# Performance work log

Measured on AMD Instinct MI355X. Metric: run time of the kernel, lower is better.

Reference implementation:

```python
import jax, jax.numpy as jnp
import numpy as np

B, S, H = 2, 2048, 2304
NH, HD, NKV = 8, 256, 4
WINDOW = 512
CAP = 50.0
THETA = 10000.0
NEG_INF = -2.3819763e38


def setup_inputs() -> dict:
    key = jax.random.key(0)
    ks = jax.random.split(key, 6)
    hidden_states = jax.random.normal(ks[0], (B, S, H), dtype=jnp.float32)
    # causal additive mask (0 where attend, -inf-ish where masked)
    i = jnp.arange(S)
    causal = i[None, :] <= i[:, None]
    attention_mask = jnp.broadcast_to(
        jnp.where(causal, 0.0, NEG_INF).astype(jnp.float32)[None, None], (B, 1, S, S)
    )
    position_ids = jnp.broadcast_to(jnp.arange(S, dtype=jnp.int32)[None], (B, S))
    scale = 0.02
    Wq = jax.random.normal(ks[1], (H, NH * HD), dtype=jnp.float32) * scale
    Wk = jax.random.normal(ks[2], (H, NKV * HD), dtype=jnp.float32) * scale
    Wv = jax.random.normal(ks[3], (H, NKV * HD), dtype=jnp.float32) * scale
    Wo = jax.random.normal(ks[4], (NH * HD, H), dtype=jnp.float32) * scale
    return {
        "hidden_states": hidden_states,
        "attention_mask": attention_mask,
        "position_ids": position_ids,
        "Wq": Wq,
        "Wk": Wk,
        "Wv": Wv,
        "Wo": Wo,
    }


def _rotate_half(x):
    h = x.shape[-1] // 2
    return jnp.concatenate([-x[..., h:], x[..., :h]], axis=-1)


def reference(hidden_states, attention_mask, position_ids, Wq, Wk, Wv, Wo):
    b, s, _ = hidden_states.shape
    q = (hidden_states @ Wq).reshape(b, s, NH, HD).transpose(0, 2, 1, 3)   # [B,NH,S,HD]
    k = (hidden_states @ Wk).reshape(b, s, NKV, HD).transpose(0, 2, 1, 3)  # [B,NKV,S,HD]
    v = (hidden_states @ Wv).reshape(b, s, NKV, HD).transpose(0, 2, 1, 3)
    # rotary embedding
    inv_freq = 1.0 / (THETA ** (jnp.arange(0, HD, 2, dtype=jnp.float32) / HD))
    freqs = position_ids.astype(jnp.float32)[..., None] * inv_freq  # [B,S,HD/2]
    emb = jnp.concatenate([freqs, freqs], axis=-1)                  # [B,S,HD]
    cos = jnp.cos(emb)[:, None]  # unsqueeze head dim
    sin = jnp.sin(emb)[:, None]
    q = q * cos + _rotate_half(q) * sin
    k = k * cos + _rotate_half(k) * sin
    # GQA: repeat kv heads
    rep = NH // NKV
    k = jnp.repeat(k, rep, axis=1)
    v = jnp.repeat(v, rep, axis=1)
    logits = jnp.einsum("bhqd,bhkd->bhqk", q, k) / jnp.sqrt(jnp.float32(HD))
    # sliding-window mask: keep |i-j| <= WINDOW-1, else NEG_INF
    idx = jnp.arange(s)
    sliding = jnp.abs(idx[:, None] - idx[None, :]) <= (WINDOW - 1)
    mask = jnp.where(sliding[None, None], attention_mask, NEG_INF)
    # tanh logit softcapping, then additive mask
    logits = jnp.tanh(logits / CAP) * CAP + mask
    probs = jax.nn.softmax(logits.astype(jnp.float32), axis=-1).astype(q.dtype)
    out = jnp.einsum("bhqk,bhkd->bhqd", probs, v)
    out = out.transpose(0, 2, 1, 3).reshape(b, s, NH * HD)
    return out @ Wo
```

## Files before the change

### kernel.cpp

```cpp
#include <hip/hip_runtime.h>
#include <cmath>

#define B_   2
#define S_   2048
#define H_   2304
#define NH_  8
#define HD_  256
#define NKV_ 4
#define WIN_ 512
#define QKVW 4096

typedef unsigned short ushort_t;
typedef __attribute__((ext_vector_type(8))) short bf16x8;
typedef __attribute__((ext_vector_type(4))) float floatx4;

__device__ __forceinline__ unsigned short f2bf(float f) {
  unsigned u = __builtin_bit_cast(unsigned, f);
  u += 0x7fff + ((u >> 16) & 1);
  return (unsigned short)(u >> 16);
}
__device__ __forceinline__ float bf2f(ushort_t v) {
  unsigned u = (unsigned)v << 16;
  return __builtin_bit_cast(float, u);
}

__device__ __forceinline__ void gl2lds16(const void* g, void* l) {
  __builtin_amdgcn_global_load_lds(
      (const __attribute__((address_space(1))) unsigned int*)g,
      (__attribute__((address_space(3))) unsigned int*)l, 16, 0, 0);
}

__global__ void cast_bf16(const float* __restrict__ in, ushort_t* __restrict__ out) {
  const int i = blockIdx.x * 256 + threadIdx.x;
  float4 v = ((const float4*)in)[i];
  ushort4 o;
  o.x = f2bf(v.x); o.y = f2bf(v.y); o.z = f2bf(v.z); o.w = f2bf(v.w);
  ((ushort4*)out)[i] = o;
}

__global__ void transpose_cast(const float* __restrict__ W, ushort_t* __restrict__ Wt,
                               int K, int N) {
  __shared__ float t[32][33];
  const int lx = threadIdx.x & 31, ly = threadIdx.x >> 5;
  const int n0 = blockIdx.x * 32, k0 = blockIdx.y * 32;
#pragma unroll
  for (int i = 0; i < 4; ++i)
    t[ly + i * 8][lx] = W[(long long)(k0 + ly + i * 8) * N + n0 + lx];
  __syncthreads();
#pragma unroll
  for (int i = 0; i < 4; ++i)
    Wt[(long long)(n0 + ly + i * 8) * K + k0 + lx] = f2bf(t[lx][ly + i * 8]);
}

#define RA(dst_, base_, qm_, kk_) do { \
  _Pragma("unroll") for (int i_ = 0; i_ < 4; ++i_) { \
    const int row_ = wm + (qm_) * 64 + i_ * 16 + l15; \
    dst_[i_] = *(const bf16x8*)&(base_)[row_ * 64 + ((((kk_) * 4 + lq) ^ (l15 & 7)) * 8)]; \
  } \
} while (0)

#define RB(dst_, base_, qn_, kk_) do { \
  _Pragma("unroll") for (int j_ = 0; j_ < 2; ++j_) { \
    const int row_ = wn + (qn_) * 32 + j_ * 16 + l15; \
    dst_[j_] = *(const bf16x8*)&(base_)[row_ * 64 + ((((kk_) * 4 + lq) ^ (l15 & 7)) * 8)]; \
  } \
} while (0)

#define MFMA8(qm_, qn_, as_, bs_) do { \
  __builtin_amdgcn_s_setprio(1); \
  _Pragma("unroll") for (int i_ = 0; i_ < 4; ++i_) \
  _Pragma("unroll") for (int j_ = 0; j_ < 2; ++j_) \
    acc[(qm_) * 4 + i_][(qn_) * 2 + j_] = __builtin_amdgcn_mfma_f32_16x16x32_bf16( \
        as_[i_], bs_[j_], acc[(qm_) * 4 + i_][(qn_) * 2 + j_], 0, 0, 0); \
  __builtin_amdgcn_s_setprio(0); \
} while (0)

#define STAGE_A(dst_, gsrc_, t_, qm_) do { \
  _Pragma("unroll") for (int jj_ = 0; jj_ < 2; ++jj_) { \
    const int g_ = w * 2 + jj_; \
    const int tr0_ = ((g_ >> 3) * 128) + (qm_) * 64 + (g_ & 7) * 8; \
    gl2lds16(gsrc_ + (size_t)tr0_ * K + (size_t)(t_) * 64 + laneOff, dst_ + tr0_ * 64); \
  } \
} while (0)

#define STAGE_B(dst_, gsrc_, t_, qn_) do { \
  _Pragma("unroll") for (int jj_ = 0; jj_ < 2; ++jj_) { \
    const int g_ = w * 2 + jj_; \
    const int tr0_ = ((g_ >> 2) * 64) + (qn_) * 32 + (g_ & 3) * 8; \
    gl2lds16(gsrc_ + (size_t)tr0_ * K + (size_t)(t_) * 64 + laneOff, dst_ + tr0_ * 64); \
  } \
} while (0)

#define SB0()  __builtin_amdgcn_sched_barrier(0)
#define BAR()  asm volatile("s_barrier" ::: "memory")
#define VM(n_) asm volatile("s_waitcnt vmcnt(" #n_ ")" ::: "memory")

#define KTILE(XA_, XB_, YA_, YB_, t_) do { \
   \
  RB(b1, XB_, 1, 0); \
  if ((t_) + 1 < NT) STAGE_A(YA_, Ab, (t_) + 1, 1); \
  MFMA8(0, 0, a0, b0); SB0(); \
   \
  RA(a1, XA_, 1, 0); \
  MFMA8(0, 1, a0, b1); SB0(); \
   \
  RA(a0, XA_, 1, 1); \
  MFMA8(1, 1, a1, b1); SB0(); \
   \
  RB(b1, XB_, 0, 1); \
  MFMA8(1, 0, a1, b0); SB0(); \
   \
  RB(b0, XB_, 1, 1); \
  MFMA8(1, 0, a0, b1); SB0(); BAR(); \
   \
  RA(a1, XA_, 0, 1); \
  if ((t_) + 2 < NT) STAGE_B(XB_, Bb, (t_) + 2, 0); \
  MFMA8(1, 1, a0, b0); \
  if ((t_) + 2 < NT) { VM(2); } else if ((t_) + 1 < NT) { VM(0); } \
  SB0(); BAR(); \
   \
  if ((t_) + 1 < NT) RA(a0, YA_, 0, 0); \
  if ((t_) + 2 < NT) STAGE_B(XB_, Bb, (t_) + 2, 1); \
  MFMA8(0, 1, a1, b0); SB0(); BAR(); \
   \
  if ((t_) + 1 < NT) RB(b0, YB_, 0, 0); \
  if ((t_) + 2 < NT) STAGE_A(XA_, Ab, (t_) + 2, 0); \
  MFMA8(0, 0, a1, b1); SB0(); \
} while (0)

template <bool OUT_BF16>
__launch_bounds__(512)
__global__ void gemm_8ph(const ushort_t* __restrict__ A,
                         const ushort_t* __restrict__ Bt,
                         void* __restrict__ Cv, int M, int N, int K) {
  extern __shared__ __attribute__((aligned(128))) ushort_t smem[];
  const int tid = threadIdx.x, lane = tid & 63, w = tid >> 6;
  const int wm = (w >> 2) * 128, wn = (w & 3) * 64;
  const int l15 = lane & 15, lq = lane >> 4;

  const int nwg  = gridDim.x * gridDim.y;
  const int orig = blockIdx.y * gridDim.x + blockIdx.x;
  const int cpx  = nwg >> 3;
  const int swz  = (orig & 7) * cpx + (orig >> 3);
  const int bx   = swz % gridDim.x, by = swz / gridDim.x;
  const int bm = by * 256, bn = bx * 256;
  const int NT = K >> 6;

  const ushort_t* Ab = A + (size_t)bm * K;
  const ushort_t* Bb = Bt + (size_t)bn * K;
  const size_t laneOff = (size_t)(lane >> 3) * K + (size_t)(((lane & 7) ^ (lane >> 3)) * 8);

  ushort_t* Ae = smem;
  ushort_t* Ao = smem + 16384;
  ushort_t* Be = smem + 32768;
  ushort_t* Bo = smem + 49152;

  floatx4 acc[8][4] = {};
  bf16x8 a0[4], a1[4], b0[2], b1[2];

  STAGE_A(Ae, Ab, 0, 0);
  STAGE_B(Be, Bb, 0, 0);
  STAGE_B(Be, Bb, 0, 1);
  STAGE_A(Ae, Ab, 0, 1);
  if (NT > 1) {
    STAGE_B(Bo, Bb, 1, 0);
    STAGE_B(Bo, Bb, 1, 1);
    STAGE_A(Ao, Ab, 1, 0);
    VM(6);
  } else {
    VM(0);
  }
  BAR();
  RA(a0, Ae, 0, 0);
  RB(b0, Be, 0, 0);

  for (int t = 0; t < NT; t += 2) {
    KTILE(Ae, Be, Ao, Bo, t);
    KTILE(Ao, Bo, Ae, Be, t + 1);
  }

  const int r0 = lq * 4;
#pragma unroll
  for (int mf = 0; mf < 8; ++mf)
#pragma unroll
    for (int nf = 0; nf < 4; ++nf) {
      const long long base = (long long)(bm + wm + mf * 16 + r0) * N + bn + wn + nf * 16 + l15;
      if (OUT_BF16) {
        ushort_t* Cp = (ushort_t*)Cv + base;
#pragma unroll
        for (int rr = 0; rr < 4; ++rr) Cp[(long long)rr * N] = f2bf(acc[mf][nf][rr]);
      } else {
        float* Cp = (float*)Cv + base;
#pragma unroll
        for (int rr = 0; rr < 4; ++rr) Cp[(long long)rr * N] = acc[mf][nf][rr];
      }
    }
}

#undef RA
#undef RB
#undef MFMA8
#undef STAGE_A
#undef STAGE_B
#undef SB0
#undef BAR
#undef VM
#undef KTILE

template <bool OUT_BF16>
__launch_bounds__(256)
__global__ void gemm_bt(const ushort_t* __restrict__ A,
                        const ushort_t* __restrict__ Bt,
                        void* __restrict__ Cv, int M, int N, int K) {
  __shared__ ushort_t As[128 * 64];
  __shared__ ushort_t Bs[128 * 64];
  const int tid = threadIdx.x, lane = tid & 63, wid = tid >> 6;
  const int bm = blockIdx.y * 128, bn = blockIdx.x * 128;
  const int wm = (wid >> 1) * 64, wn = (wid & 1) * 64;

  floatx4 acc[4][4] = {};

  const int r  = tid >> 1;
  const int cp = (tid & 1) * 4;
  const int wkey = r & 7;
  const ushort_t* Ap = A  + (long long)(bm + r) * K + cp * 8;
  const ushort_t* Bp = Bt + (long long)(bn + r) * K + cp * 8;
  ushort_t* Aw = &As[r * 64];
  ushort_t* Bw = &Bs[r * 64];

  const int l15 = lane & 15, lq = lane >> 4;
  const int rkey = l15 & 7;

  bf16x8 ar[4], br[4];
#pragma unroll
  for (int i = 0; i < 4; ++i) {
    ar[i] = *(const bf16x8*)(Ap + i * 8);
    br[i] = *(const bf16x8*)(Bp + i * 8);
  }

  for (int k0 = 0; k0 < K; k0 += 64) {
    __syncthreads();
#pragma unroll
    for (int i = 0; i < 4; ++i) {
      *(bf16x8*)&Aw[((cp + i) ^ wkey) * 8] = ar[i];
      *(bf16x8*)&Bw[((cp + i) ^ wkey) * 8] = br[i];
    }
    __syncthreads();

    if (k0 + 64 < K) {
      const int kn = k0 + 64;
#pragma unroll
      for (int i = 0; i < 4; ++i) {
        ar[i] = *(const bf16x8*)(Ap + kn + i * 8);
        br[i] = *(const bf16x8*)(Bp + kn + i * 8);
      }
    }

#pragma unroll
    for (int kk = 0; kk < 2; ++kk) {
      bf16x8 af[4], bfr[4];
#pragma unroll
      for (int i = 0; i < 4; ++i) {
        af[i]  = *(const bf16x8*)&As[(wm + i * 16 + l15) * 64 + ((kk * 4 + lq) ^ rkey) * 8];
        bfr[i] = *(const bf16x8*)&Bs[(wn + i * 16 + l15) * 64 + ((kk * 4 + lq) ^ rkey) * 8];
      }
#pragma unroll
      for (int i = 0; i < 4; ++i)
#pragma unroll
        for (int j = 0; j < 4; ++j)
          acc[i][j] = __builtin_amdgcn_mfma_f32_16x16x32_bf16(af[i], bfr[j], acc[i][j], 0, 0, 0);
    }
  }

  const int r0 = lq * 4, c0 = l15;
#pragma unroll
  for (int i = 0; i < 4; ++i)
#pragma unroll
    for (int j = 0; j < 4; ++j) {
      const long long base = (long long)(bm + wm + i * 16 + r0) * N + bn + wn + j * 16 + c0;
      if (OUT_BF16) {
        ushort_t* Cp = (ushort_t*)Cv + base;
#pragma unroll
        for (int rr = 0; rr < 4; ++rr) Cp[(long long)rr * N] = f2bf(acc[i][j][rr]);
      } else {
        float* Cp = (float*)Cv + base;
#pragma unroll
        for (int rr = 0; rr < 4; ++rr) Cp[(long long)rr * N] = acc[i][j][rr];
      }
    }
}

__global__ void rope_inplace(ushort_t* __restrict__ QKV16, const int* __restrict__ pos) {
  const int bs  = blockIdx.x;
  const int gid = blockIdx.y * 256 + threadIdx.x;
  const int head = gid >> 7;
  const int d    = gid & 127;
  const float pp   = (float)pos[bs];
  const float invf = __expf(-(float)d * (9.210340371976184f / 128.0f));
  const float ang  = pp * invf;
  float sn, cc;
  __sincosf(ang, &sn, &cc);
  ushort_t* base = QKV16 + (size_t)bs * QKVW + head * HD_;
  const float x1 = bf2f(base[d]);
  const float x2 = bf2f(base[d + 128]);
  float o1 = x1 * cc - x2 * sn;
  float o2 = x2 * cc + x1 * sn;
  if (head < NH_) { o1 *= 0.0625f; o2 *= 0.0625f; }
  base[d]       = f2bf(o1);
  base[d + 128] = f2bf(o2);
}

__global__ void v_prep(const ushort_t* __restrict__ QKV16, ushort_t* __restrict__ Vt16) {
  __shared__ ushort_t tile[32][33];
  const int k0 = blockIdx.x * 32, d0 = blockIdx.y * 32;
  const int b = blockIdx.z >> 2, hk = blockIdx.z & 3;
  const int lx = threadIdx.x & 31, ly = threadIdx.x >> 5;
#pragma unroll
  for (int i = 0; i < 4; ++i)
    tile[ly + 8 * i][lx] =
        QKV16[(size_t)(b * S_ + k0 + ly + 8 * i) * QKVW + 3072 + hk * HD_ + d0 + lx];
  __syncthreads();
#pragma unroll
  for (int i = 0; i < 4; ++i)
    Vt16[((size_t)(b * NKV_ + hk) * HD_ + d0 + ly + 8 * i) * S_ + k0 + lx] =
        tile[lx][ly + 8 * i];
}

__launch_bounds__(512)
__global__ void attn_mfma(const ushort_t* __restrict__ QKV16,
                          const ushort_t* __restrict__ Vt16,
                          ushort_t* __restrict__ AOb) {
  __shared__ ushort_t Ks[32 * 256];
  __shared__ ushort_t Vts[256 * 32];
  __shared__ ushort_t Ps[8][16 * 32];
  __shared__ float rsb[8][16];

  const int lane = threadIdx.x & 63, w = threadIdx.x >> 6;
  const int l15 = lane & 15, lq = lane >> 4;
  const int qb = blockIdx.x * 64;
  const int hp = blockIdx.y, b = blockIdx.z;
  const int h  = hp * 2 + (w >> 2);
  const int hw = w & 3;

  const ushort_t* Qh = QKV16 + (size_t)b * S_ * QKVW + h * HD_;
  const ushort_t* Kh = QKV16 + (size_t)b * S_ * QKVW + 2048 + hp * HD_;
  const ushort_t* Vh = Vt16 + ((size_t)(b * NKV_ + hp) * HD_) * S_;

  const int qw = qb + hw * 16;

  bf16x8 afq[8];
  {
    const ushort_t* qr = Qh + (size_t)(qw + l15) * QKVW + lq * 8;
#pragma unroll
    for (int kd = 0; kd < 8; ++kd) afq[kd] = *(const bf16x8*)(qr + kd * 32);
  }

  floatx4 acc[16] = {};
  float rs[4] = {0.f, 0.f, 0.f, 0.f};

  int kb0 = qb - (WIN_ - 1);
  if (kb0 < 0) kb0 = 0;
  kb0 &= ~31;

  const int ksp = lane & 31, ksr = lane >> 5;
  const int vsp = lane & 3,  vsr = lane >> 2;

  for (int kb = kb0; kb < qb + 64; kb += 32) {
    __syncthreads();
#pragma unroll
    for (int i = 0; i < 2; ++i) {
      const int kl = w * 4 + 2 * i + ksr;
      gl2lds16(Kh + (size_t)(kb + kl) * QKVW + (ksp ^ (kl & 31)) * 8,
               &Ks[(w * 4 + 2 * i) * 256]);
    }
#pragma unroll
    for (int i = 0; i < 2; ++i) {
      const int dl = w * 32 + 16 * i + vsr;
      gl2lds16(Vh + (size_t)dl * S_ + kb + (vsp ^ ((dl >> 1) & 3)) * 8,
               &Vts[(w * 32 + 16 * i) * 32]);
    }
    __syncthreads();

    if (kb <= qw + 15 && kb + 31 >= qw - (WIN_ - 1)) {
      ushort_t* Pw = Ps[w];
#pragma unroll
      for (int kt = 0; kt < 2; ++kt) {
        floatx4 sacc = {};
        const int keyl = kt * 16 + l15;
        const int krow = keyl * 256;
        const int ksw = keyl & 31;
#pragma unroll
        for (int kd = 0; kd < 8; ++kd) {
          bf16x8 bk = *(const bf16x8*)&Ks[krow + ((kd * 4 + lq) ^ ksw) * 8];
          sacc = __builtin_amdgcn_mfma_f32_16x16x32_bf16(afq[kd], bk, sacc, 0, 0, 0);
        }
        const int keyg = kb + keyl;
#pragma unroll
        for (int rr = 0; rr < 4; ++rr) {
          const int qg = qw + lq * 4 + rr;
          const float t = __expf(sacc[rr] * 0.04f);
          const float L = 50.f - __fdividef(100.f, t + 1.f);
          float p = __expf(L);
          p = (keyg <= qg && keyg >= qg - (WIN_ - 1)) ? p : 0.f;
          rs[rr] += p;
          const int ql = lq * 4 + rr;
          const int ch = kt * 2 + (l15 >> 3);
          Pw[ql * 32 + ((ch ^ ((ql >> 1) & 3)) * 8) + (l15 & 7)] = f2bf(p);
        }
      }
      asm volatile("s_waitcnt lgkmcnt(0)" ::: "memory");

      const bf16x8 bp = *(const bf16x8*)&Pw[l15 * 32 + ((lq ^ ((l15 >> 1) & 3)) * 8)];
      const int vsw = (l15 >> 1) & 3;
#pragma unroll
      for (int t = 0; t < 16; ++t) {
        bf16x8 av = *(const bf16x8*)&Vts[(t * 16 + l15) * 32 + ((lq ^ vsw) * 8)];
        acc[t] = __builtin_amdgcn_mfma_f32_16x16x32_bf16(av, bp, acc[t], 0, 0, 0);
      }
    }
  }

#pragma unroll
  for (int rr = 0; rr < 4; ++rr) {
    rs[rr] += __shfl_xor(rs[rr], 1, 64);
    rs[rr] += __shfl_xor(rs[rr], 2, 64);
    rs[rr] += __shfl_xor(rs[rr], 4, 64);
    rs[rr] += __shfl_xor(rs[rr], 8, 64);
  }
  if (l15 == 0) {
#pragma unroll
    for (int rr = 0; rr < 4; ++rr) rsb[w][lq * 4 + rr] = rs[rr];
  }
  asm volatile("s_waitcnt lgkmcnt(0)" ::: "memory");
  __builtin_amdgcn_wave_barrier();
  const float inv = 1.0f / rsb[w][l15];

  const size_t ob = ((size_t)(b * S_ + qw + l15) * NH_ + h) * HD_;
#pragma unroll
  for (int t = 0; t < 16; ++t) {
    ushort4 o;
    o.x = f2bf(acc[t][0] * inv);
    o.y = f2bf(acc[t][1] * inv);
    o.z = f2bf(acc[t][2] * inv);
    o.w = f2bf(acc[t][3] * inv);
    *(ushort4*)&AOb[ob + t * 16 + lq * 4] = o;
  }
}

extern "C" void kernel_launch(void* const* d_in, const int* in_sizes, int n_in,
                              void* d_out, int out_size, void* d_ws, size_t ws_size,
                              hipStream_t stream) {
  const float* X   = (const float*)d_in[0];
  const int*   pos = (const int*)d_in[2];
  const float* Wq  = (const float*)d_in[3];
  const float* Wk  = (const float*)d_in[4];
  const float* Wv  = (const float*)d_in[5];
  const float* Wo  = (const float*)d_in[6];
  float* out = (float*)d_out;

  const int M  = B_ * S_;
  const int NQ = NH_ * HD_;
  const int NK = NKV_ * HD_;

  char* w = (char*)d_ws;
  ushort_t* QKV16 = (ushort_t*)w;  w += (size_t)M * QKVW * 2;
  ushort_t* Xb    = (ushort_t*)w;  w += (size_t)M * H_ * 2;
  ushort_t* Wqkvt = (ushort_t*)w;  w += (size_t)QKVW * H_ * 2;
  ushort_t* Wot   = (ushort_t*)w;  w += (size_t)H_ * NQ * 2;
  ushort_t* Vt16  = (ushort_t*)w;  w += (size_t)B_ * NKV_ * S_ * HD_ * 2;
  ushort_t* AOb   = (ushort_t*)w;  w += (size_t)M * NQ * 2;

  static bool g_init = false, g_8ph_ok = false;
  if (!g_init) {
    hipError_t e1 = hipFuncSetAttribute(
        reinterpret_cast<const void*>(&gemm_8ph<true>),
        hipFuncAttributeMaxDynamicSharedMemorySize, 131072);
    g_8ph_ok = (e1 == hipSuccess);
    g_init = true;
  }

  dim3 blk(256);

  cast_bf16<<<(M * H_) / 1024, blk, 0, stream>>>(X, Xb);
  transpose_cast<<<dim3(NQ / 32, H_ / 32), blk, 0, stream>>>(Wq, Wqkvt, H_, NQ);
  transpose_cast<<<dim3(NK / 32, H_ / 32), blk, 0, stream>>>(Wk, Wqkvt + (size_t)2048 * H_, H_, NK);
  transpose_cast<<<dim3(NK / 32, H_ / 32), blk, 0, stream>>>(Wv, Wqkvt + (size_t)3072 * H_, H_, NK);
  transpose_cast<<<dim3(H_ / 32, NQ / 32), blk, 0, stream>>>(Wo, Wot, NQ, H_);

  if (g_8ph_ok) {
    gemm_8ph<true><<<dim3(QKVW / 256, M / 256), dim3(512), 131072, stream>>>(
        Xb, Wqkvt, QKV16, M, QKVW, H_);
  } else {
    gemm_bt<true><<<dim3(QKVW / 128, M / 128), blk, 0, stream>>>(Xb, Wqkvt, QKV16, M, QKVW, H_);
  }

  rope_inplace<<<dim3(M, 6), blk, 0, stream>>>(QKV16, pos);
  v_prep<<<dim3(S_ / 32, HD_ / 32, B_ * NKV_), blk, 0, stream>>>(QKV16, Vt16);

  attn_mfma<<<dim3(S_ / 64, NKV_, B_), dim3(512), 0, stream>>>(QKV16, Vt16, AOb);

  gemm_bt<false><<<dim3(H_ / 128, M / 128), blk, 0, stream>>>(AOb, Wot, out, M, H_, NQ);
}
```

Before: 349.1 us.

## Restructure QKV GEMM into triple-buffered 32-wide K tiles with staggered wave groups

The 256x256 QKV GEMM now uses K tiles of 32 instead of 64, with three LDS buffers in place of two. Global-to-LDS prefetch runs two tiles ahead. The two halves of the workgroup run the MFMA quadrants in opposite orders, so their LDS reads and MFMA bursts interleave. LDS use drops from 128KB to 96KB, and the phase-specific waits are replaced by a single vmcnt(0) plus barrier per tile. The cost is twice as many barrier and full-wait points per unit of K, which may reduce latency hiding.

```diff
diff --git a/kernel.cpp b/kernel.cpp
--- a/kernel.cpp
+++ b/kernel.cpp
@@ -52,17 +52,17 @@
     Wt[(long long)(n0 + ly + i * 8) * K + k0 + lx] = f2bf(t[lx][ly + i * 8]);
 }
 
-#define RA(dst_, base_, qm_, kk_) do { \
+#define RA32(dst_, base_, qm_) do { \
   _Pragma("unroll") for (int i_ = 0; i_ < 4; ++i_) { \
     const int row_ = wm + (qm_) * 64 + i_ * 16 + l15; \
-    dst_[i_] = *(const bf16x8*)&(base_)[row_ * 64 + ((((kk_) * 4 + lq) ^ (l15 & 7)) * 8)]; \
+    dst_[i_] = *(const bf16x8*)&(base_)[row_ * 32 + ((lq ^ (row_ & 3)) * 8)]; \
   } \
 } while (0)
 
-#define RB(dst_, base_, qn_, kk_) do { \
+#define RB32(dst_, base_, qn_) do { \
   _Pragma("unroll") for (int j_ = 0; j_ < 2; ++j_) { \
     const int row_ = wn + (qn_) * 32 + j_ * 16 + l15; \
-    dst_[j_] = *(const bf16x8*)&(base_)[row_ * 64 + ((((kk_) * 4 + lq) ^ (l15 & 7)) * 8)]; \
+    dst_[j_] = *(const bf16x8*)&(base_)[row_ * 32 + ((lq ^ (row_ & 3)) * 8)]; \
   } \
 } while (0)
 
@@ -75,57 +75,51 @@
   __builtin_amdgcn_s_setprio(0); \
 } while (0)
 
-#define STAGE_A(dst_, gsrc_, t_, qm_) do { \
-  _Pragma("unroll") for (int jj_ = 0; jj_ < 2; ++jj_) { \
-    const int g_ = w * 2 + jj_; \
-    const int tr0_ = ((g_ >> 3) * 128) + (qm_) * 64 + (g_ & 7) * 8; \
-    gl2lds16(gsrc_ + (size_t)tr0_ * K + (size_t)(t_) * 64 + laneOff, dst_ + tr0_ * 64); \
-  } \
-} while (0)
-
-#define STAGE_B(dst_, gsrc_, t_, qn_) do { \
-  _Pragma("unroll") for (int jj_ = 0; jj_ < 2; ++jj_) { \
-    const int g_ = w * 2 + jj_; \
-    const int tr0_ = ((g_ >> 2) * 64) + (qn_) * 32 + (g_ & 3) * 8; \
-    gl2lds16(gsrc_ + (size_t)tr0_ * K + (size_t)(t_) * 64 + laneOff, dst_ + tr0_ * 64); \
-  } \
+#define STG32(dst_, gsrc_, t_, hf_) do { \
+  const int r0_ = (hf_) * 128 + w * 16; \
+  gl2lds16(gsrc_ + (size_t)r0_ * K + (size_t)(t_) * 32 + laneOff, dst_ + r0_ * 32); \
 } while (0)
 
 #define SB0()  __builtin_amdgcn_sched_barrier(0)
 #define BAR()  asm volatile("s_barrier" ::: "memory")
-#define VM(n_) asm volatile("s_waitcnt vmcnt(" #n_ ")" ::: "memory")
-
-#define KTILE(XA_, XB_, YA_, YB_, t_) do { \
-   \
-  RB(b1, XB_, 1, 0); \
-  if ((t_) + 1 < NT) STAGE_A(YA_, Ab, (t_) + 1, 1); \
-  MFMA8(0, 0, a0, b0); SB0(); \
-   \
-  RA(a1, XA_, 1, 0); \
-  MFMA8(0, 1, a0, b1); SB0(); \
-   \
-  RA(a0, XA_, 1, 1); \
-  MFMA8(1, 1, a1, b1); SB0(); \
-   \
-  RB(b1, XB_, 0, 1); \
-  MFMA8(1, 0, a1, b0); SB0(); \
-   \
-  RB(b0, XB_, 1, 1); \
-  MFMA8(1, 0, a0, b1); SB0(); BAR(); \
-   \
-  RA(a1, XA_, 0, 1); \
-  if ((t_) + 2 < NT) STAGE_B(XB_, Bb, (t_) + 2, 0); \
-  MFMA8(1, 1, a0, b0); \
-  if ((t_) + 2 < NT) { VM(2); } else if ((t_) + 1 < NT) { VM(0); } \
-  SB0(); BAR(); \
-   \
-  if ((t_) + 1 < NT) RA(a0, YA_, 0, 0); \
-  if ((t_) + 2 < NT) STAGE_B(XB_, Bb, (t_) + 2, 1); \
-  MFMA8(0, 1, a1, b0); SB0(); BAR(); \
-   \
-  if ((t_) + 1 < NT) RB(b0, YB_, 0, 0); \
-  if ((t_) + 2 < NT) STAGE_A(XA_, Ab, (t_) + 2, 0); \
-  MFMA8(0, 0, a1, b1); SB0(); \
+#define VM0()  asm volatile("s_waitcnt vmcnt(0)" ::: "memory")
+
+#define KT(XA_, XB_, YA_, YB_, ZA_, ZB_, t_) do { \
+  const bool st_ = (t_) + 2 < NT, cr_ = (t_) + 1 < NT; \
+  if (grpE) { \
+     \
+    RB32(bQ, XB_, 1); \
+    if (st_) { STG32(ZA_, Ab, (t_) + 2, 0); STG32(ZA_, Ab, (t_) + 2, 1); } \
+    SB0(); MFMA8(0, 0, aP, bP); SB0(); \
+     \
+    RA32(aQ, XA_, 1); \
+    if (st_) { STG32(ZB_, Bb, (t_) + 2, 0); STG32(ZB_, Bb, (t_) + 2, 1); } \
+    SB0(); MFMA8(0, 1, aP, bQ); SB0(); \
+     \
+    if (cr_) RA32(aP, YA_, 0); \
+    SB0(); MFMA8(1, 1, aQ, bQ); SB0(); \
+     \
+    MFMA8(1, 0, aQ, bP); SB0(); \
+    if (cr_) RB32(bP, YB_, 0); \
+    SB0(); \
+  } else { \
+     \
+    RB32(bQ, XB_, 0); \
+    if (st_) { STG32(ZA_, Ab, (t_) + 2, 0); STG32(ZA_, Ab, (t_) + 2, 1); } \
+    SB0(); MFMA8(1, 1, aP, bP); SB0(); \
+     \
+    RA32(aQ, XA_, 0); \
+    if (st_) { STG32(ZB_, Bb, (t_) + 2, 0); STG32(ZB_, Bb, (t_) + 2, 1); } \
+    SB0(); MFMA8(1, 0, aP, bQ); SB0(); \
+     \
+    if (cr_) RA32(aP, YA_, 1); \
+    SB0(); MFMA8(0, 0, aQ, bQ); SB0(); \
+     \
+    MFMA8(0, 1, aQ, bP); SB0(); \
+    if (cr_) RB32(bP, YB_, 1); \
+    SB0(); \
+  } \
+  VM0(); BAR(); \
 } while (0)
 
 template <bool OUT_BF16>
@@ -137,6 +131,7 @@
   const int tid = threadIdx.x, lane = tid & 63, w = tid >> 6;
   const int wm = (w >> 2) * 128, wn = (w & 3) * 64;
   const int l15 = lane & 15, lq = lane >> 4;
+  const bool grpE = (w < 4);
 
   const int nwg  = gridDim.x * gridDim.y;
   const int orig = blockIdx.y * gridDim.x + blockIdx.x;
@@ -144,39 +139,36 @@
   const int swz  = (orig & 7) * cpx + (orig >> 3);
   const int bx   = swz % gridDim.x, by = swz / gridDim.x;
   const int bm = by * 256, bn = bx * 256;
-  const int NT = K >> 6;
+  const int NT = K >> 5;
 
   const ushort_t* Ab = A + (size_t)bm * K;
   const ushort_t* Bb = Bt + (size_t)bn * K;
-  const size_t laneOff = (size_t)(lane >> 3) * K + (size_t)(((lane & 7) ^ (lane >> 3)) * 8);
-
-  ushort_t* Ae = smem;
-  ushort_t* Ao = smem + 16384;
-  ushort_t* Be = smem + 32768;
-  ushort_t* Bo = smem + 49152;
+  const size_t laneOff = (size_t)(lane >> 2) * K + (size_t)((((lane & 3) ^ ((lane >> 2) & 3))) * 8);
+
+  ushort_t* A0_ = smem;
+  ushort_t* A1_ = smem + 8192;
+  ushort_t* A2_ = smem + 16384;
+  ushort_t* B0_ = smem + 24576;
+  ushort_t* B1_ = smem + 32768;
+  ushort_t* B2_ = smem + 40960;
 
   floatx4 acc[8][4] = {};
-  bf16x8 a0[4], a1[4], b0[2], b1[2];
-
-  STAGE_A(Ae, Ab, 0, 0);
-  STAGE_B(Be, Bb, 0, 0);
-  STAGE_B(Be, Bb, 0, 1);
-  STAGE_A(Ae, Ab, 0, 1);
+  bf16x8 aP[4], aQ[4], bP[2], bQ[2];
+
+  STG32(A0_, Ab, 0, 0); STG32(A0_, Ab, 0, 1);
+  STG32(B0_, Bb, 0, 0); STG32(B0_, Bb, 0, 1);
   if (NT > 1) {
-    STAGE_B(Bo, Bb, 1, 0);
-    STAGE_B(Bo, Bb, 1, 1);
-    STAGE_A(Ao, Ab, 1, 0);
-    VM(6);
-  } else {
-    VM(0);
-  }
-  BAR();
-  RA(a0, Ae, 0, 0);
-  RB(b0, Be, 0, 0);
-
-  for (int t = 0; t < NT; t += 2) {
-    KTILE(Ae, Be, Ao, Bo, t);
-    KTILE(Ao, Bo, Ae, Be, t + 1);
+    STG32(A1_, Ab, 1, 0); STG32(A1_, Ab, 1, 1);
+    STG32(B1_, Bb, 1, 0); STG32(B1_, Bb, 1, 1);
+  }
+  VM0(); BAR();
+  if (grpE) { RA32(aP, A0_, 0); RB32(bP, B0_, 0); }
+  else      { RA32(aP, A0_, 1); RB32(bP, B0_, 1); }
+
+  for (int t = 0; t < NT; t += 3) {
+    KT(A0_, B0_, A1_, B1_, A2_, B2_, t);
+    KT(A1_, B1_, A2_, B2_, A0_, B0_, t + 1);
+    KT(A2_, B2_, A0_, B0_, A1_, B1_, t + 2);
   }
 
   const int r0 = lq * 4;
@@ -197,15 +189,14 @@
     }
 }
 
-#undef RA
-#undef RB
+#undef RA32
+#undef RB32
 #undef MFMA8
-#undef STAGE_A
-#undef STAGE_B
+#undef STG32
 #undef SB0
 #undef BAR
-#undef VM
-#undef KTILE
+#undef VM0
+#undef KT
 
 template <bool OUT_BF16>
 __launch_bounds__(256)
@@ -474,7 +465,7 @@
   if (!g_init) {
     hipError_t e1 = hipFuncSetAttribute(
         reinterpret_cast<const void*>(&gemm_8ph<true>),
-        hipFuncAttributeMaxDynamicSharedMemorySize, 131072);
+        hipFuncAttributeMaxDynamicSharedMemorySize, 98304);
     g_8ph_ok = (e1 == hipSuccess);
     g_init = true;
   }
@@ -488,7 +479,7 @@
   transpose_cast<<<dim3(H_ / 32, NQ / 32), blk, 0, stream>>>(Wo, Wot, NQ, H_);
 
   if (g_8ph_ok) {
-    gemm_8ph<true><<<dim3(QKVW / 256, M / 256), dim3(512), 131072, stream>>>(
+    gemm_8ph<true><<<dim3(QKVW / 256, M / 256), dim3(512), 98304, stream>>>(
         Xb, Wqkvt, QKV16, M, QKVW, H_);
   } else {
     gemm_bt<true><<<dim3(QKVW / 128, M / 128), blk, 0, stream>>>(Xb, Wqkvt, QKV16, M, QKVW, H_);
```

After: 714.2 us. +104.6%, slower.

## Restructure 8-phase GEMM pipeline to load full K-halves per quadrant with barriers

Applied to the files above, without the earlier changes.

Replaces the register-double-buffered KTILE schedule (a0/a1, b0/b1 ping-pong across k-halves) with a schedule that loads both k-substeps of each A/B quadrant into registers at once and runs 16 MFMAs per quadrant. Each phase is wrapped in explicit workgroup barriers and lgkmcnt waits, and global-to-LDS staging is re-sequenced with vmcnt(4). The aim is a simpler, more regular schedule with fewer LDS-read/MFMA interleaving hazards. The added barriers per phase may serialize LDS reads and MFMA work and reduce overlap.

```diff
diff --git a/kernel.cpp b/kernel.cpp
--- a/kernel.cpp
+++ b/kernel.cpp
@@ -52,26 +52,29 @@
     Wt[(long long)(n0 + ly + i * 8) * K + k0 + lx] = f2bf(t[lx][ly + i * 8]);
 }
 
-#define RA(dst_, base_, qm_, kk_) do { \
+#define RA(base_, qm_) do { \
   _Pragma("unroll") for (int i_ = 0; i_ < 4; ++i_) { \
     const int row_ = wm + (qm_) * 64 + i_ * 16 + l15; \
-    dst_[i_] = *(const bf16x8*)&(base_)[row_ * 64 + ((((kk_) * 4 + lq) ^ (l15 & 7)) * 8)]; \
+    _Pragma("unroll") for (int kk_ = 0; kk_ < 2; ++kk_) \
+      a[i_][kk_] = *(const bf16x8*)&(base_)[row_ * 64 + (((kk_ * 4 + lq) ^ (l15 & 7)) * 8)]; \
   } \
 } while (0)
 
-#define RB(dst_, base_, qn_, kk_) do { \
+#define RB(base_, qn_) do { \
   _Pragma("unroll") for (int j_ = 0; j_ < 2; ++j_) { \
     const int row_ = wn + (qn_) * 32 + j_ * 16 + l15; \
-    dst_[j_] = *(const bf16x8*)&(base_)[row_ * 64 + ((((kk_) * 4 + lq) ^ (l15 & 7)) * 8)]; \
+    _Pragma("unroll") for (int kk_ = 0; kk_ < 2; ++kk_) \
+      b[j_][kk_] = *(const bf16x8*)&(base_)[row_ * 64 + (((kk_ * 4 + lq) ^ (l15 & 7)) * 8)]; \
   } \
 } while (0)
 
-#define MFMA8(qm_, qn_, as_, bs_) do { \
+#define MFMAQ(qm_, qn_) do { \
   __builtin_amdgcn_s_setprio(1); \
+  _Pragma("unroll") for (int kk_ = 0; kk_ < 2; ++kk_) \
   _Pragma("unroll") for (int i_ = 0; i_ < 4; ++i_) \
   _Pragma("unroll") for (int j_ = 0; j_ < 2; ++j_) \
     acc[(qm_) * 4 + i_][(qn_) * 2 + j_] = __builtin_amdgcn_mfma_f32_16x16x32_bf16( \
-        as_[i_], bs_[j_], acc[(qm_) * 4 + i_][(qn_) * 2 + j_], 0, 0, 0); \
+        a[i_][kk_], b[j_][kk_], acc[(qm_) * 4 + i_][(qn_) * 2 + j_], 0, 0, 0); \
   __builtin_amdgcn_s_setprio(0); \
 } while (0)
 
@@ -91,42 +94,11 @@
   } \
 } while (0)
 
-#define SB0()  __builtin_amdgcn_sched_barrier(0)
-#define BAR()  asm volatile("s_barrier" ::: "memory")
-#define VM(n_) asm volatile("s_waitcnt vmcnt(" #n_ ")" ::: "memory")
-
-#define KTILE(XA_, XB_, YA_, YB_, t_) do { \
-   \
-  RB(b1, XB_, 1, 0); \
-  if ((t_) + 1 < NT) STAGE_A(YA_, Ab, (t_) + 1, 1); \
-  MFMA8(0, 0, a0, b0); SB0(); \
-   \
-  RA(a1, XA_, 1, 0); \
-  MFMA8(0, 1, a0, b1); SB0(); \
-   \
-  RA(a0, XA_, 1, 1); \
-  MFMA8(1, 1, a1, b1); SB0(); \
-   \
-  RB(b1, XB_, 0, 1); \
-  MFMA8(1, 0, a1, b0); SB0(); \
-   \
-  RB(b0, XB_, 1, 1); \
-  MFMA8(1, 0, a0, b1); SB0(); BAR(); \
-   \
-  RA(a1, XA_, 0, 1); \
-  if ((t_) + 2 < NT) STAGE_B(XB_, Bb, (t_) + 2, 0); \
-  MFMA8(1, 1, a0, b0); \
-  if ((t_) + 2 < NT) { VM(2); } else if ((t_) + 1 < NT) { VM(0); } \
-  SB0(); BAR(); \
-   \
-  if ((t_) + 1 < NT) RA(a0, YA_, 0, 0); \
-  if ((t_) + 2 < NT) STAGE_B(XB_, Bb, (t_) + 2, 1); \
-  MFMA8(0, 1, a1, b0); SB0(); BAR(); \
-   \
-  if ((t_) + 1 < NT) RB(b0, YB_, 0, 0); \
-  if ((t_) + 2 < NT) STAGE_A(XA_, Ab, (t_) + 2, 0); \
-  MFMA8(0, 0, a1, b1); SB0(); \
-} while (0)
+#define SB0()   __builtin_amdgcn_sched_barrier(0)
+#define BARR()  do { SB0(); __builtin_amdgcn_s_barrier(); } while (0)
+#define LGKM0() do { asm volatile("s_waitcnt lgkmcnt(0)" ::: "memory"); SB0(); } while (0)
+#define LGKM8() asm volatile("s_waitcnt lgkmcnt(8)" ::: "memory")
+#define VM(n_)  asm volatile("s_waitcnt vmcnt(" #n_ ")" ::: "memory")
 
 template <bool OUT_BF16>
 __launch_bounds__(512)
@@ -156,27 +128,81 @@
   ushort_t* Bo = smem + 49152;
 
   floatx4 acc[8][4] = {};
-  bf16x8 a0[4], a1[4], b0[2], b1[2];
+  bf16x8 a[4][2], b[2][2];
 
   STAGE_A(Ae, Ab, 0, 0);
-  STAGE_B(Be, Bb, 0, 0);
   STAGE_B(Be, Bb, 0, 1);
   STAGE_A(Ae, Ab, 0, 1);
-  if (NT > 1) {
-    STAGE_B(Bo, Bb, 1, 0);
-    STAGE_B(Bo, Bb, 1, 1);
-    STAGE_A(Ao, Ab, 1, 0);
-    VM(6);
-  } else {
-    VM(0);
-  }
-  BAR();
-  RA(a0, Ae, 0, 0);
-  RB(b0, Be, 0, 0);
+  STAGE_B(Be, Bb, 0, 0);
+  STAGE_A(Ao, Ab, 1, 0);
+  STAGE_B(Bo, Bb, 1, 1);
+  VM(4);
+  BARR();
 
   for (int t = 0; t < NT; t += 2) {
-    KTILE(Ae, Be, Ao, Bo, t);
-    KTILE(Ao, Bo, Ae, Be, t + 1);
+    const bool more = (t + 2 < NT);
+
+    RA(Ae, 0); RB(Be, 0);
+    STAGE_A(Ao, Ab, t + 1, 1);
+    LGKM8();
+    BARR();
+    LGKM0();
+    MFMAQ(0, 0);
+    BARR();
+
+    RB(Be, 1);
+    STAGE_B(Bo, Bb, t + 1, 0);
+    BARR();
+    LGKM0();
+    MFMAQ(0, 1);
+    BARR();
+
+    RA(Ae, 1);
+    if (more) STAGE_A(Ae, Ab, t + 2, 0);
+    BARR();
+    LGKM0();
+    MFMAQ(1, 1);
+    BARR();
+
+    RB(Be, 0);
+    if (more) STAGE_B(Be, Bb, t + 2, 1);
+    BARR();
+    LGKM0();
+    MFMAQ(1, 0);
+    SB0();
+    if (more) { VM(4); } else { VM(0); }
+    BARR();
+
+    RA(Ao, 0); RB(Bo, 0);
+    if (more) STAGE_A(Ae, Ab, t + 2, 1);
+    LGKM8();
+    BARR();
+    LGKM0();
+    MFMAQ(0, 0);
+    BARR();
+
+    RB(Bo, 1);
+    if (more) STAGE_B(Be, Bb, t + 2, 0);
+    BARR();
+    LGKM0();
+    MFMAQ(0, 1);
+    BARR();
+
+    RA(Ao, 1);
+    if (more) STAGE_A(Ao, Ab, t + 3, 0);
+    BARR();
+    LGKM0();
+    MFMAQ(1, 1);
+    BARR();
+
+    RB(Bo, 0);
+    if (more) STAGE_B(Bo, Bb, t + 3, 1);
+    BARR();
+    LGKM0();
+    MFMAQ(1, 0);
+    SB0();
+    if (more) { VM(4); } else { VM(0); }
+    BARR();
   }
 
   const int r0 = lq * 4;
@@ -199,13 +225,14 @@
 
 #undef RA
 #undef RB
-#undef MFMA8
+#undef MFMAQ
 #undef STAGE_A
 #undef STAGE_B
 #undef SB0
-#undef BAR
+#undef BARR
+#undef LGKM0
+#undef LGKM8
 #undef VM
-#undef KTILE
 
 template <bool OUT_BF16>
 __launch_bounds__(256)
```

Result: slower. 361.0 us (+3.4%).
